# Optimization experiments

Hardware: AMD Instinct MI355X
Metric: run time of the kernel (lower is better)

Reference implementation:

```python
import jax, jax.numpy as jnp
import numpy as np

T, D, F, E, K = 2048, 512, 2048, 8, 2


def setup_inputs() -> dict:
    key = jax.random.key(0)
    ks = jax.random.split(key, 5)
    scaled = lambda k, shape, fan: jax.random.normal(k, shape, jnp.float32) * (fan ** -0.5)
    x = jax.random.normal(ks[0], (T, D), jnp.float32)
    Wg = scaled(ks[1], (D, E), D)          # gate: Linear(D -> E), no bias
    W1 = scaled(ks[2], (E, D, F), D)       # per-expert up proj
    W3 = scaled(ks[3], (E, D, F), D)       # per-expert gate proj (SwiGLU)
    W2 = scaled(ks[4], (E, F, D), F)       # per-expert down proj
    return {"x": x, "Wg": Wg, "W1": W1, "W2": W2, "W3": W3}


def reference(x, Wg, W1, W2, W3):
    # gate logits + top-k routing (topk over raw logits, softmax over the k picked logits,
    # computed in float32 then cast back -- matches the torch source)
    logits = x @ Wg                                   # [T, E]
    topw, sel = jax.lax.top_k(logits, K)              # [T, K] each
    weights = jax.nn.softmax(topw.astype(jnp.float32), axis=-1).astype(x.dtype)
    out = jnp.zeros_like(x)
    # NOTE: the source uses `output[batch_idx] = ...` (assignment, not +=), so later
    # experts OVERWRITE earlier ones for tokens routed to multiple experts.
    # We replicate that exactly with sequential jnp.where overwrites.
    for i in range(E):
        hit = sel == i                                # [T, K]
        mask = hit.any(axis=-1)                       # [T] tokens routed to expert i
        w_i = jnp.sum(jnp.where(hit, weights, 0.0), axis=-1)  # [T] routing weight
        h = jax.nn.silu(x @ W1[i]) * (x @ W3[i])      # [T, F] SwiGLU
        y = h @ W2[i]                                 # [T, D]
        out = jnp.where(mask[:, None], w_i[:, None] * y, out)
    return out
```

## Files before the change

kernel.cpp:

```cpp
#include <hip/hip_runtime.h>
#include <hip/hip_bf16.h>
#include <math.h>

typedef __attribute__((ext_vector_type(8))) short short8;
typedef __attribute__((ext_vector_type(4))) float f32x4;

#define T_TOK 2048
#define D_DIM 512
#define F_DIM 2048
#define E_NUM 8
#define MAXT1 40

__device__ __forceinline__ unsigned short f2bf(float f) {
  union { float f; unsigned u; } c; c.f = f;
  unsigned u = c.u;
  return (unsigned short)((u + 0x7fffu + ((u >> 16) & 1u)) >> 16);
}

__device__ __forceinline__ void gld16(const void* g, void* l) {
  __builtin_amdgcn_global_load_lds((const __attribute__((address_space(1))) int*)g,
                                   (__attribute__((address_space(3))) int*)l, 16, 0, 0);
}

__global__ __launch_bounds__(256) void k_prep(const float* __restrict__ xin,
                                              const float* __restrict__ Wg,
                                              const float* __restrict__ W1,
                                              const float* __restrict__ W3,
                                              const float* __restrict__ W2,
                                              int* __restrict__ jbuf,
                                              float* __restrict__ wbuf,
                                              unsigned short* __restrict__ xb,
                                              unsigned short* __restrict__ w1f,
                                              unsigned short* __restrict__ w3f,
                                              unsigned short* __restrict__ w2f) {
  __shared__ float4 tile4[64 * 32];
  int bz = blockIdx.x, tid = threadIdx.x;

  if (bz < 256) {
    int gid = bz * 256 + tid;
    int t = gid >> 5, seg = gid & 31;
    const float* xp = xin + (size_t)t * D_DIM + seg * 16;
    unsigned short* xo = xb + (size_t)t * D_DIM + seg * 16;
    float acc[8];
#pragma unroll
    for (int e = 0; e < 8; ++e) acc[e] = 0.f;
#pragma unroll
    for (int i = 0; i < 4; ++i) {
      float4 v = *(const float4*)(xp + i * 4);
      ushort4 o;
      o.x = f2bf(v.x); o.y = f2bf(v.y); o.z = f2bf(v.z); o.w = f2bf(v.w);
      *(ushort4*)(xo + i * 4) = o;
      const float* xs = (const float*)&v;
#pragma unroll
      for (int q = 0; q < 4; ++q) {
        int d = seg * 16 + i * 4 + q;
        const float4* wr = (const float4*)(Wg + (size_t)d * 8);
        float4 w0 = wr[0], w1 = wr[1];
        acc[0] += xs[q] * w0.x; acc[1] += xs[q] * w0.y;
        acc[2] += xs[q] * w0.z; acc[3] += xs[q] * w0.w;
        acc[4] += xs[q] * w1.x; acc[5] += xs[q] * w1.y;
        acc[6] += xs[q] * w1.z; acc[7] += xs[q] * w1.w;
      }
    }
#pragma unroll
    for (int off = 1; off < 32; off <<= 1)
#pragma unroll
      for (int e = 0; e < 8; ++e) acc[e] += __shfl_xor(acc[e], off);
    if (seg == 0) {
      float l0 = -1e30f, l1 = -1e30f; int i0 = 0, i1 = 0;
#pragma unroll
      for (int e = 0; e < 8; ++e) {
        float l = acc[e];
        if (l > l0) { l1 = l0; i1 = i0; l0 = l; i0 = e; }
        else if (l > l1) { l1 = l; i1 = e; }
      }
      int j; float w;
      if (i0 > i1) { j = i0; w = 1.f / (1.f + expf(l1 - l0)); }
      else         { j = i1; w = 1.f / (1.f + expf(l0 - l1)); }
      jbuf[t] = j; wbuf[t] = w;
    }
    return;
  }

  const float* in; unsigned short* out;
  int K, N, n0, k0;
  if (bz < 2304) {
    int idx = bz - 256;
    int z = idx >> 7, rem = idx & 127;
    K = 512; N = 2048;
    n0 = (rem & 15) * 128; k0 = (rem >> 4) * 64;
    size_t zsz = (size_t)(K / 32) * (N / 16) * 512;
    if (z < 8) { in = W1 + (size_t)z * K * N;       out = w1f + (size_t)z * zsz; }
    else       { in = W3 + (size_t)(z - 8) * K * N; out = w3f + (size_t)(z - 8) * zsz; }
  } else {
    int idx = bz - 2304;
    int z = idx >> 7, rem = idx & 127;
    K = 2048; N = 512;
    n0 = (rem & 3) * 128; k0 = (rem >> 2) * 64;
    size_t zsz = (size_t)(K / 32) * (N / 16) * 512;
    in = W2 + (size_t)z * K * N; out = w2f + (size_t)z * zsz;
  }
  {
    int lr = tid >> 5, lc = tid & 31;
#pragma unroll
    for (int it = 0; it < 8; ++it) {
      int row = it * 8 + lr;
      float4 v = *(const float4*)(in + (size_t)(k0 + row) * N + n0 + lc * 4);
      tile4[row * 32 + ((lc + (row >> 3) * 4) & 31)] = v;
    }
  }
  __syncthreads();
  const float* tf = (const float*)tile4;
  int wv = tid >> 6, l = tid & 63;
  int n4l = (l & 15) >> 2, nr = l & 3, kg = (l >> 4) * 8;
#pragma unroll
  for (int q = 0; q < 4; ++q) {
    int fid = wv * 4 + q;
    int nb = fid >> 1, kb = fid & 1;
    int n4 = nb * 4 + n4l;
    short8 o;
#pragma unroll
    for (int j = 0; j < 8; ++j) {
      int k = kb * 32 + kg + j;
      int slot = k * 32 + ((n4 + (k >> 3) * 4) & 31);
      o[j] = (short)f2bf(tf[slot * 4 + nr]);
    }
    unsigned short* op = out + (((size_t)(n0 / 16 + nb) * (K / 32)) + (k0 / 32 + kb)) * 512 + l * 8;
    *(short8*)op = o;
  }
}

__global__ __launch_bounds__(256) void k_bucket(const int* __restrict__ jbuf,
                                                int* __restrict__ cntp,
                                                int* __restrict__ basep,
                                                int* __restrict__ list,
                                                int* __restrict__ tl1,
                                                int* __restrict__ ntl) {
  __shared__ int scnt[8], scur[8];
  int tid = threadIdx.x;
  if (tid < 8) scnt[tid] = 0;
  __syncthreads();
  for (int t = tid; t < T_TOK; t += 256) atomicAdd(&scnt[jbuf[t]], 1);
  __syncthreads();
  if (tid == 0) {
    int run = 0;
    for (int e = 0; e < 8; ++e) {
      cntp[e] = scnt[e]; basep[e] = run; scur[e] = run;
      run += scnt[e];
    }
    int n1 = 0, bb = 0;
    for (int e = 0; e < 8; ++e) {
      for (int m = 0; m < scnt[e]; m += 64) tl1[n1++] = (e << 16) | (bb + m);
      bb += scnt[e];
    }
    ntl[0] = n1;
  }
  __syncthreads();
  for (int t = tid; t < T_TOK; t += 256) {
    int j = jbuf[t];
    int p = atomicAdd(&scur[j], 1);
    list[p] = t;
  }
}

__global__ __launch_bounds__(256, 2) void k_ffn1(const unsigned short* __restrict__ xb,
                                                 const unsigned short* __restrict__ w1f,
                                                 const unsigned short* __restrict__ w3f,
                                                 const int* __restrict__ cntp,
                                                 const int* __restrict__ basep,
                                                 const int* __restrict__ list,
                                                 const int* __restrict__ tl1,
                                                 const int* __restrict__ ntl,
                                                 unsigned short* __restrict__ hbuf) {
  int L = blockIdx.x;
  int b = (L & 7) * 80 + (L >> 3);
  int x = b % 40, y = b / 40;
  if (x >= ntl[0]) return;
  int pk = tl1[x];
  int e = pk >> 16, g0 = pk & 0xffff;
  int lim = basep[e] + cntp[e];
  __shared__ unsigned short sA[64 * 512];
  int tid = threadIdx.x, wv = tid >> 6, l = tid & 63;
  int wr = wv >> 1, wc = wv & 1;

#pragma unroll
  for (int it = 0; it < 16; ++it) {
    int row = wv * 16 + it;
    int gr = g0 + row; if (gr >= lim) gr = lim - 1;
    int tok = list[gr];
    int slot = (l & 56) | ((l & 7) ^ (row & 7));
    gld16(xb + (size_t)tok * D_DIM + slot * 8, sA + row * 512);
  }

  const unsigned short* w1b = w1f + ((size_t)(e * 128 + y * 8 + wc) * 16) * 512 + l * 8;
  const unsigned short* w3b = w3f + ((size_t)(e * 128 + y * 8 + wc) * 16) * 512 + l * 8;

  short8 P1[8], P3[8], Q1[8], Q3[8];
  auto loadS = [&](short8* r1, short8* r3, int s) {
    int g = s >> 1, h = s & 1;
    const unsigned short* p1 = w1b + ((size_t)(g * 32 + h * 8)) * 512;
    const unsigned short* p3 = w3b + ((size_t)(g * 32 + h * 8)) * 512;
#pragma unroll
    for (int q = 0; q < 8; ++q) {
      r1[q] = *(const short8*)(p1 + (size_t)q * 512);
      r3[q] = *(const short8*)(p3 + (size_t)q * 512);
    }
  };

  f32x4 au[2], av[2];
  auto halfC = [&](const short8* r1, const short8* r3, int h) {
#pragma unroll
    for (int q = 0; q < 8; ++q) {
      int kf = h * 8 + q;
      short8 a[2];
#pragma unroll
      for (int i = 0; i < 2; ++i) {
        int r = wr * 32 + i * 16 + (l & 15);
        int slot = kf * 4 + (l >> 4);
        int swz = (slot & 56) | ((slot & 7) ^ (r & 7));
        a[i] = *(const short8*)(sA + r * 512 + swz * 8);
      }
#pragma unroll
      for (int i = 0; i < 2; ++i) {
        au[i] = __builtin_amdgcn_mfma_f32_16x16x32_bf16(a[i], r1[q], au[i], 0, 0, 0);
        av[i] = __builtin_amdgcn_mfma_f32_16x16x32_bf16(a[i], r3[q], av[i], 0, 0, 0);
      }
    }
  };

  loadS(P1, P3, 0);
  __syncthreads();

  int cloc = l & 15, rb = (l >> 4) * 4;
#pragma unroll
  for (int gp = 0; gp < 4; ++gp) {
#pragma unroll
    for (int i = 0; i < 2; ++i) {
      au[i] = (f32x4){0.f, 0.f, 0.f, 0.f};
      av[i] = (f32x4){0.f, 0.f, 0.f, 0.f};
    }
    loadS(Q1, Q3, gp * 2 + 1);
    halfC(P1, P3, 0);
    if (gp < 3) loadS(P1, P3, gp * 2 + 2);
    halfC(Q1, Q3, 1);
    int col = (y * 4 + gp) * 32 + wc * 16 + cloc;
#pragma unroll
    for (int i = 0; i < 2; ++i)
#pragma unroll
      for (int r = 0; r < 4; ++r) {
        int gr = g0 + wr * 32 + i * 16 + rb + r;
        if (gr < lim) {
          float uu = au[i][r], vv = av[i][r];
          float hh = (uu / (1.f + expf(-uu))) * vv;
          hbuf[(size_t)gr * F_DIM + col] = f2bf(hh);
        }
      }
  }
}

__global__ __launch_bounds__(256, 3) void k_ffn2(const unsigned short* __restrict__ hbuf,
                                                 const unsigned short* __restrict__ w2f,
                                                 const int* __restrict__ cntp,
                                                 const int* __restrict__ basep,
                                                 const int* __restrict__ list,
                                                 const int* __restrict__ tl1,
                                                 const int* __restrict__ ntl,
                                                 const float* __restrict__ wbuf,
                                                 float* __restrict__ out) {
  int L = blockIdx.x;
  int c = L & 7, q = L >> 3;
  int x = c * 5 + (q % 5);
  int nt = q / 5;
  if (x >= ntl[0]) return;
  int pk = tl1[x];
  int e = pk >> 16, g0 = pk & 0xffff;
  int lim = basep[e] + cntp[e];
  __shared__ unsigned short sA[2 * 8192];
  int tid = threadIdx.x, wv = tid >> 6, l = tid & 63;
  int wr = wv >> 1, wc = wv & 1;

  auto stage = [&](int buf, int ck) {
#pragma unroll
    for (int it = 0; it < 4; ++it) {
      int row0 = it * 16 + wv * 4;
      int row = row0 + (l >> 4);
      int gr = g0 + row; if (gr > T_TOK - 1) gr = T_TOK - 1;
      int sl = (l & 8) | ((l & 7) ^ (row & 7));
      gld16(hbuf + (size_t)gr * F_DIM + ck * 128 + sl * 8, sA + buf * 8192 + row0 * 128);
    }
  };

  const unsigned short* b2p = w2f + ((size_t)(e * 32 + nt * 2 + wc) * 64) * 512 + l * 8;

  short8 Ba[4], Bb[4];
  auto loadB = [&](short8* B, int ck) {
#pragma unroll
    for (int kk = 0; kk < 4; ++kk)
      B[kk] = *(const short8*)(b2p + (size_t)(ck * 4 + kk) * 512);
  };

  f32x4 acc[2];
  acc[0] = (f32x4){0.f, 0.f, 0.f, 0.f};
  acc[1] = (f32x4){0.f, 0.f, 0.f, 0.f};

  auto compute = [&](const short8* B, int cur) {
#pragma unroll
    for (int kk = 0; kk < 4; ++kk) {
      short8 a[2];
#pragma unroll
      for (int i = 0; i < 2; ++i) {
        int r = wr * 32 + i * 16 + (l & 15);
        int slot = kk * 4 + (l >> 4);
        int swz = (slot & 8) | ((slot & 7) ^ (r & 7));
        a[i] = *(const short8*)(sA + cur * 8192 + r * 128 + swz * 8);
      }
      acc[0] = __builtin_amdgcn_mfma_f32_16x16x32_bf16(a[0], B[kk], acc[0], 0, 0, 0);
      acc[1] = __builtin_amdgcn_mfma_f32_16x16x32_bf16(a[1], B[kk], acc[1], 0, 0, 0);
    }
  };

  stage(0, 0);
  loadB(Ba, 0);
  __syncthreads();
  int cur = 0;
  for (int ck = 0; ck < 16; ck += 2) {
    stage(cur ^ 1, ck + 1);
    loadB(Bb, ck + 1);
    compute(Ba, cur);
    __syncthreads();
    cur ^= 1;
    if (ck + 2 < 16) {
      stage(cur ^ 1, ck + 2);
      loadB(Ba, ck + 2);
    }
    compute(Bb, cur);
    __syncthreads();
    cur ^= 1;
  }

  int cloc = l & 15, rb = (l >> 4) * 4;
#pragma unroll
  for (int i = 0; i < 2; ++i)
#pragma unroll
    for (int r = 0; r < 4; ++r) {
      int gr = g0 + wr * 32 + i * 16 + rb + r;
      if (gr < lim) {
        int tok = list[gr];
        out[(size_t)tok * D_DIM + nt * 32 + wc * 16 + cloc] = wbuf[tok] * acc[i][r];
      }
    }
}

extern "C" void kernel_launch(void* const* d_in, const int* in_sizes, int n_in,
                              void* d_out, int out_size, void* d_ws, size_t ws_size,
                              hipStream_t stream) {
  const float* x  = (const float*)d_in[0];
  const float* Wg = (const float*)d_in[1];
  const float* W1 = (const float*)d_in[2];
  const float* W2 = (const float*)d_in[3];
  const float* W3 = (const float*)d_in[4];
  float* out = (float*)d_out;
  char* ws = (char*)d_ws;

  int*            jbuf  = (int*)(ws + 0);
  float*          wbuf  = (float*)(ws + 8192);
  int*            cntp  = (int*)(ws + 16384);
  int*            basep = (int*)(ws + 16448);
  int*            list  = (int*)(ws + 16640);
  int*            tl1   = (int*)(ws + 24832);
  int*            ntl   = (int*)(ws + 25600);
  unsigned short* xb    = (unsigned short*)(ws + 32768);
  unsigned short* w1f   = (unsigned short*)(ws + 32768 + 2097152);
  unsigned short* w3f   = (unsigned short*)(ws + 32768 + 2097152 + 16777216);
  unsigned short* w2f   = (unsigned short*)(ws + 32768 + 2097152 + 2 * 16777216);
  unsigned short* hbuf  = (unsigned short*)(ws + 32768 + 2097152 + 3 * 16777216);

  k_prep<<<dim3(3328), dim3(256), 0, stream>>>(x, Wg, W1, W3, W2, jbuf, wbuf, xb, w1f, w3f, w2f);
  k_bucket<<<dim3(1), dim3(256), 0, stream>>>(jbuf, cntp, basep, list, tl1, ntl);
  k_ffn1<<<dim3(640), dim3(256), 0, stream>>>(xb, w1f, w3f, cntp, basep, list, tl1, ntl, hbuf);
  k_ffn2<<<dim3(640), dim3(256), 0, stream>>>(hbuf, w2f, cntp, basep, list, tl1, ntl, wbuf, out);
}
```

Before: 82.87 us.

## Move W2 bf16 repack from prep kernel into FFN1 launch

The W2 fp32-to-bf16 fragment repack is taken out of the prep kernel and appended as extra blocks (index 640 and up) of the first expert FFN kernel. The repack can then run alongside the FFN1 GEMM blocks instead of serialising ahead of routing and bucketing, which shortens the critical path. The cost is that FFN1 now shares CUs with bandwidth-heavy repack blocks and carries a larger grid. The repack blocks also reuse the GEMM shared buffer, so their occupancy is bounded by the GEMM's LDS footprint.

```diff
diff --git a/kernel.cpp b/kernel.cpp
--- a/kernel.cpp
+++ b/kernel.cpp
@@ -26,13 +26,11 @@
                                               const float* __restrict__ Wg,
                                               const float* __restrict__ W1,
                                               const float* __restrict__ W3,
-                                              const float* __restrict__ W2,
                                               int* __restrict__ jbuf,
                                               float* __restrict__ wbuf,
                                               unsigned short* __restrict__ xb,
                                               unsigned short* __restrict__ w1f,
-                                              unsigned short* __restrict__ w3f,
-                                              unsigned short* __restrict__ w2f) {
+                                              unsigned short* __restrict__ w3f) {
   __shared__ float4 tile4[64 * 32];
   int bz = blockIdx.x, tid = threadIdx.x;
 
@@ -82,24 +80,14 @@
     return;
   }
 
+  int idx = bz - 256;
+  int z = idx >> 7, rem = idx & 127;
+  const int K = 512, N = 2048;
+  int n0 = (rem & 15) * 128, k0 = (rem >> 4) * 64;
+  size_t zsz = (size_t)(K / 32) * (N / 16) * 512;
   const float* in; unsigned short* out;
-  int K, N, n0, k0;
-  if (bz < 2304) {
-    int idx = bz - 256;
-    int z = idx >> 7, rem = idx & 127;
-    K = 512; N = 2048;
-    n0 = (rem & 15) * 128; k0 = (rem >> 4) * 64;
-    size_t zsz = (size_t)(K / 32) * (N / 16) * 512;
-    if (z < 8) { in = W1 + (size_t)z * K * N;       out = w1f + (size_t)z * zsz; }
-    else       { in = W3 + (size_t)(z - 8) * K * N; out = w3f + (size_t)(z - 8) * zsz; }
-  } else {
-    int idx = bz - 2304;
-    int z = idx >> 7, rem = idx & 127;
-    K = 2048; N = 512;
-    n0 = (rem & 3) * 128; k0 = (rem >> 2) * 64;
-    size_t zsz = (size_t)(K / 32) * (N / 16) * 512;
-    in = W2 + (size_t)z * K * N; out = w2f + (size_t)z * zsz;
-  }
+  if (z < 8) { in = W1 + (size_t)z * K * N;       out = w1f + (size_t)z * zsz; }
+  else       { in = W3 + (size_t)(z - 8) * K * N; out = w3f + (size_t)(z - 8) * zsz; }
   {
     int lr = tid >> 5, lc = tid & 31;
 #pragma unroll
@@ -163,15 +151,59 @@
   }
 }
 
-__global__ __launch_bounds__(256, 2) void k_ffn1(const unsigned short* __restrict__ xb,
-                                                 const unsigned short* __restrict__ w1f,
-                                                 const unsigned short* __restrict__ w3f,
-                                                 const int* __restrict__ cntp,
-                                                 const int* __restrict__ basep,
-                                                 const int* __restrict__ list,
-                                                 const int* __restrict__ tl1,
-                                                 const int* __restrict__ ntl,
-                                                 unsigned short* __restrict__ hbuf) {
+__global__ __launch_bounds__(256, 2) void k_ffn1w2(const unsigned short* __restrict__ xb,
+                                                   const unsigned short* __restrict__ w1f,
+                                                   const unsigned short* __restrict__ w3f,
+                                                   const float* __restrict__ W2,
+                                                   unsigned short* __restrict__ w2f,
+                                                   const int* __restrict__ cntp,
+                                                   const int* __restrict__ basep,
+                                                   const int* __restrict__ list,
+                                                   const int* __restrict__ tl1,
+                                                   const int* __restrict__ ntl,
+                                                   unsigned short* __restrict__ hbuf) {
+  __shared__ unsigned short sA[64 * 512];
+  int tid = threadIdx.x, wv = tid >> 6, l = tid & 63;
+
+  if (blockIdx.x >= 640) {
+    int idx = blockIdx.x - 640;
+    int z = idx >> 7, rem = idx & 127;
+    const int K = 2048, N = 512;
+    int n0 = (rem & 3) * 128, k0 = (rem >> 2) * 64;
+    size_t zsz = (size_t)(K / 32) * (N / 16) * 512;
+    const float* in = W2 + (size_t)z * K * N;
+    unsigned short* out = w2f + (size_t)z * zsz;
+    float4* tile4 = (float4*)sA;
+    {
+      int lr = tid >> 5, lc = tid & 31;
+#pragma unroll
+      for (int it = 0; it < 8; ++it) {
+        int row = it * 8 + lr;
+        float4 v = *(const float4*)(in + (size_t)(k0 + row) * N + n0 + lc * 4);
+        tile4[row * 32 + ((lc + (row >> 3) * 4) & 31)] = v;
+      }
+    }
+    __syncthreads();
+    const float* tf = (const float*)tile4;
+    int n4l = (l & 15) >> 2, nr = l & 3, kg = (l >> 4) * 8;
+#pragma unroll
+    for (int q = 0; q < 4; ++q) {
+      int fid = wv * 4 + q;
+      int nb = fid >> 1, kb = fid & 1;
+      int n4 = nb * 4 + n4l;
+      short8 o;
+#pragma unroll
+      for (int j = 0; j < 8; ++j) {
+        int k = kb * 32 + kg + j;
+        int slot = k * 32 + ((n4 + (k >> 3) * 4) & 31);
+        o[j] = (short)f2bf(tf[slot * 4 + nr]);
+      }
+      unsigned short* op = out + (((size_t)(n0 / 16 + nb) * (K / 32)) + (k0 / 32 + kb)) * 512 + l * 8;
+      *(short8*)op = o;
+    }
+    return;
+  }
+
   int L = blockIdx.x;
   int b = (L & 7) * 80 + (L >> 3);
   int x = b % 40, y = b / 40;
@@ -179,8 +211,6 @@
   int pk = tl1[x];
   int e = pk >> 16, g0 = pk & 0xffff;
   int lim = basep[e] + cntp[e];
-  __shared__ unsigned short sA[64 * 512];
-  int tid = threadIdx.x, wv = tid >> 6, l = tid & 63;
   int wr = wv >> 1, wc = wv & 1;
 
 #pragma unroll
@@ -375,8 +405,8 @@
   unsigned short* w2f   = (unsigned short*)(ws + 32768 + 2097152 + 2 * 16777216);
   unsigned short* hbuf  = (unsigned short*)(ws + 32768 + 2097152 + 3 * 16777216);
 
-  k_prep<<<dim3(3328), dim3(256), 0, stream>>>(x, Wg, W1, W3, W2, jbuf, wbuf, xb, w1f, w3f, w2f);
+  k_prep<<<dim3(2304), dim3(256), 0, stream>>>(x, Wg, W1, W3, jbuf, wbuf, xb, w1f, w3f);
   k_bucket<<<dim3(1), dim3(256), 0, stream>>>(jbuf, cntp, basep, list, tl1, ntl);
-  k_ffn1<<<dim3(640), dim3(256), 0, stream>>>(xb, w1f, w3f, cntp, basep, list, tl1, ntl, hbuf);
+  k_ffn1w2<<<dim3(1664), dim3(256), 0, stream>>>(xb, w1f, w3f, W2, w2f, cntp, basep, list, tl1, ntl, hbuf);
   k_ffn2<<<dim3(640), dim3(256), 0, stream>>>(hbuf, w2f, cntp, basep, list, tl1, ntl, wbuf, out);
 }
```

New measurement: 79.82 us. -3.7%, faster.
